# Kernel optimization log

Hardware: AMD Instinct MI355X
Metric: run time of the kernel (lower is better)

Reference implementation:

```python
import jax, jax.numpy as jnp
import numpy as np

HEADS = 12
D_MODEL = 768
D_K = D_MODEL // HEADS
BS, SEQ = 2, 4096


def setup_inputs() -> dict:
    key = jax.random.key(0)
    ks = jax.random.split(key, 12)
    s = 1.0 / np.sqrt(D_MODEL)
    return {
        "q": jax.random.normal(ks[0], (BS, SEQ, D_MODEL), jnp.float32),
        "k": jax.random.normal(ks[1], (BS, SEQ, D_MODEL), jnp.float32),
        "v": jax.random.normal(ks[2], (BS, SEQ, D_MODEL), jnp.float32),
        "Wq": jax.random.normal(ks[3], (D_MODEL, D_MODEL), jnp.float32) * s,
        "bq": jax.random.normal(ks[4], (D_MODEL,), jnp.float32) * s,
        "Wk": jax.random.normal(ks[5], (D_MODEL, D_MODEL), jnp.float32) * s,
        "bk": jax.random.normal(ks[6], (D_MODEL,), jnp.float32) * s,
        "Wv": jax.random.normal(ks[7], (D_MODEL, D_MODEL), jnp.float32) * s,
        "bv": jax.random.normal(ks[8], (D_MODEL,), jnp.float32) * s,
        "Wo": jax.random.normal(ks[9], (D_MODEL, D_MODEL), jnp.float32) * s,
        "bo": jax.random.normal(ks[10], (D_MODEL,), jnp.float32) * s,
        "mask": jnp.ones((BS, 1, SEQ), jnp.int32),
    }


def reference(q, k, v, Wq, bq, Wk, bk, Wv, bv, Wo, bo, mask):
    bs, sq, _ = q.shape
    # torch Linear: x @ W.T + b; then reshape to (bs, S, h, d_k) and transpose to (bs, h, S, d_k)
    def proj(x, W, b):
        y = x @ W.T + b
        return y.reshape(bs, -1, HEADS, D_K).transpose(0, 2, 1, 3)
    qh, kh, vh = proj(q, Wq, bq), proj(k, Wk, bk), proj(v, Wv, bv)
    scores = jnp.einsum("bhqd,bhkd->bhqk", qh, kh) / np.sqrt(D_K)
    # mask.unsqueeze(1): [bs,1,1,S_kv], masked_fill where mask == 0
    scores = jnp.where(mask[:, None, :, :] == 0, jnp.float32(-1e9), scores)
    attn = jax.nn.softmax(scores, axis=-1)  # dropout = identity (eval mode)
    ctx = jnp.einsum("bhqk,bhkd->bhqd", attn, vh)
    concat = ctx.transpose(0, 2, 1, 3).reshape(bs, sq, D_MODEL)
    return concat @ Wo.T + bo
```

## Files before the change

kernel.cpp:

```cpp
#include <hip/hip_runtime.h>
#include <hip/hip_bf16.h>

typedef __bf16 bf16x8 __attribute__((ext_vector_type(8)));
typedef __bf16 bf16x4 __attribute__((ext_vector_type(4)));
typedef short s16x4 __attribute__((ext_vector_type(4)));
typedef float f32x4 __attribute__((ext_vector_type(4)));
typedef unsigned short u16;

#define HEADS 12
#define DK 64
#define DM 768
#define SEQL 4096
#define BSZ 2
#define MROWS (BSZ * SEQL)
#define WELEM (DM * DM)
#define NX 6291456
#define WTOT (4 * WELEM)
#define BTOT (4 * 768)

#define QSCALE 0.180336880434245f
#define EXP2F(x) __builtin_amdgcn_exp2f(x)

__device__ __forceinline__ float bf2f(u16 x) {
    unsigned int u = ((unsigned int)x) << 16;
    return __uint_as_float(u);
}
__device__ __forceinline__ u16 f2bf(float f) {
    unsigned int u = __float_as_uint(f);
    u += 0x7fff + ((u >> 16) & 1);
    return (u16)(u >> 16);
}
__device__ __forceinline__ unsigned int cvt_pk(float lo, float hi) {
#if __has_builtin(__builtin_amdgcn_cvt_pk_bf16_f32)
    auto r = __builtin_amdgcn_cvt_pk_bf16_f32(lo, hi);
    unsigned int u;
    __builtin_memcpy(&u, &r, 4);
    return u;
#else
    return (unsigned int)f2bf(lo) | ((unsigned int)f2bf(hi) << 16);
#endif
}

__global__ void detect_dtype(const u16* __restrict__ q, int* __restrict__ flag) {
    __shared__ int cnt;
    if (threadIdx.x == 0) cnt = 0;
    __syncthreads();
    int c = 0;
    for (int i = threadIdx.x; i < 16384; i += 256) {
        u16 x = q[i];
        if (((x >> 7) & 0xFF) == 0xFF) c++;
    }
    if (c) atomicAdd(&cnt, c);
    __syncthreads();
    if (threadIdx.x == 0) *flag = (cnt > 0) ? 1 : 0;
}

__global__ __launch_bounds__(256) void convert_x(
    const void* __restrict__ X0, const void* __restrict__ X1, const void* __restrict__ X2,
    u16* __restrict__ Xc, const int* __restrict__ flag) {
    const int f32m = *flag;
    int i8 = blockIdx.x * 256 + threadIdx.x;
    if (i8 >= 3 * NX / 8) return;
    int w = i8 / (NX / 8);
    int off8 = i8 - w * (NX / 8);
    const void* src = (w == 0) ? X0 : (w == 1) ? X1 : X2;
    u16* dst = Xc + (size_t)w * NX + (size_t)off8 * 8;
    if (f32m) {
        float4 f0 = ((const float4*)src)[off8 * 2];
        float4 f1 = ((const float4*)src)[off8 * 2 + 1];
        uint4 p = {cvt_pk(f0.x, f0.y), cvt_pk(f0.z, f0.w),
                   cvt_pk(f1.x, f1.y), cvt_pk(f1.z, f1.w)};
        *(uint4*)dst = p;
    } else {
        *(uint4*)dst = ((const uint4*)src)[off8];
    }
}

__global__ __launch_bounds__(256) void convert_wb(
    const void* __restrict__ W0, const void* __restrict__ W1,
    const void* __restrict__ W2, const void* __restrict__ W3,
    const void* __restrict__ B0, const void* __restrict__ B1,
    const void* __restrict__ B2, const void* __restrict__ B3,
    u16* __restrict__ Wc, u16* __restrict__ bc, const int* __restrict__ flag) {
    const int f32m = *flag;
    int i4 = blockIdx.x * 256 + threadIdx.x;
    const int n4 = (WTOT + BTOT) / 4;
    if (i4 >= n4) return;
    int base = i4 * 4;
    const void* src;
    u16* dst;
    int off;
    if (base < WTOT) {
        int w = base / WELEM;
        off = base - w * WELEM;
        src = (w == 0) ? W0 : (w == 1) ? W1 : (w == 2) ? W2 : W3;
        dst = Wc + w * WELEM + off;
    } else {
        int bi = base - WTOT;
        int w = bi / 768;
        off = bi - w * 768;
        src = (w == 0) ? B0 : (w == 1) ? B1 : (w == 2) ? B2 : B3;
        dst = bc + w * 768 + off;
    }
    if (f32m) {
        float4 f = *(const float4*)((const float*)src + off);
        uint2 p = {cvt_pk(f.x, f.y), cvt_pk(f.z, f.w)};
        *(uint2*)dst = p;
    } else {
        *(uint2*)dst = *(const uint2*)((const u16*)src + off);
    }
}

typedef __attribute__((address_space(1))) unsigned int glb_u32;
typedef __attribute__((address_space(3))) unsigned int lds_u32;

__device__ __forceinline__ void gld16(const u16* g, u16* l) {
    __builtin_amdgcn_global_load_lds((glb_u32*)g, (lds_u32*)l, 16, 0, 0);
}

template <int NCH>
__device__ __forceinline__ void stage_g(const u16* gbase, u16* lbase, int tid) {
#pragma unroll
    for (int it = 0; it < NCH / 256; ++it) {
        int c = it * 256 + tid;
        int row = c >> 2, p = c & 3;
        int gc = p ^ (row & 3);
        gld16(gbase + (size_t)row * DM + gc * 8, lbase + c * 8);
    }
}

__global__ __launch_bounds__(256) void gemm_qkv3(
    const u16* __restrict__ Xc, const u16* __restrict__ Wc, const u16* __restrict__ bc,
    u16* __restrict__ Yq, u16* __restrict__ Yk, u16* __restrict__ Yv) {
    __shared__ __align__(16) u16 As[2][128 * 32];
    __shared__ __align__(16) u16 Bs[2][128 * 32];

    const int by  = blockIdx.y;
    const int sel = by / 6;
    const int n0  = (by - sel * 6) * 128;
    const int m0  = blockIdx.x * 128;

    const u16* X  = Xc + (size_t)sel * NX;
    const u16* W  = Wc + (size_t)sel * WELEM;
    const u16* Bp = bc + sel * 768;
    u16* Y = sel == 0 ? Yq : (sel == 1 ? Yk : Yv);
    const float oscale = sel == 0 ? QSCALE : 1.0f;

    const int tid = threadIdx.x, lane = tid & 63, wave = tid >> 6;
    const int wr = (wave >> 1) * 64, wc2 = (wave & 1) * 64;
    const int l15 = lane & 15, quad = lane >> 4;
    const int ck = (quad ^ (l15 & 3)) * 8;

    f32x4 acc[4][4] = {};

    stage_g<512>(X + (size_t)m0 * DM, &As[0][0], tid);
    stage_g<512>(W + (size_t)n0 * DM, &Bs[0][0], tid);
    __syncthreads();

    for (int it = 0; it < 24; ++it) {
        const int cur = it & 1, nxt = cur ^ 1;
        if (it < 23) {
            stage_g<512>(X + (size_t)m0 * DM + (it + 1) * 32, &As[nxt][0], tid);
            stage_g<512>(W + (size_t)n0 * DM + (it + 1) * 32, &Bs[nxt][0], tid);
        }
        bf16x8 a[4], b[4];
#pragma unroll
        for (int i = 0; i < 4; ++i)
            a[i] = *(const bf16x8*)&As[cur][(wr + i * 16 + l15) * 32 + ck];
#pragma unroll
        for (int j = 0; j < 4; ++j)
            b[j] = *(const bf16x8*)&Bs[cur][(wc2 + j * 16 + l15) * 32 + ck];
#pragma unroll
        for (int i = 0; i < 4; ++i)
#pragma unroll
            for (int j = 0; j < 4; ++j)
                acc[i][j] = __builtin_amdgcn_mfma_f32_16x16x32_bf16(a[i], b[j], acc[i][j], 0, 0, 0);
        __syncthreads();
    }

#pragma unroll
    for (int j = 0; j < 4; ++j) {
        int o = n0 + wc2 + j * 16 + l15;
        float bv = bf2f(Bp[o]);
        int h = o >> 6, d = o & 63;
#pragma unroll
        for (int i = 0; i < 4; ++i) {
            int row0 = m0 + wr + i * 16 + quad * 4;
            int bb = row0 >> 12, s0 = row0 & (SEQL - 1);
            if (sel < 2) {
#pragma unroll
                for (int r = 0; r < 4; ++r)
                    Y[((bb * HEADS + h) << 18) + ((s0 + r) << 6) + d] =
                        f2bf((acc[i][j][r] + bv) * oscale);
            } else {
                uint2 p = {cvt_pk(acc[i][j][0] + bv, acc[i][j][1] + bv),
                           cvt_pk(acc[i][j][2] + bv, acc[i][j][3] + bv)};
                *(uint2*)&Y[((bb * HEADS + h) << 18) + (d << 12) + s0] = p;
            }
        }
    }
}

__global__ __launch_bounds__(256) void gemm_out3(const u16* __restrict__ X,
                                                 const u16* __restrict__ W,
                                                 const u16* __restrict__ Bp,
                                                 void* __restrict__ Y,
                                                 const int* __restrict__ flag) {
    __shared__ __align__(16) u16 As[2][64 * 32];
    __shared__ __align__(16) u16 Bs[2][128 * 32];

    const int f32mode = *flag;
    const int m0 = blockIdx.x * 64, n0 = blockIdx.y * 128;
    const int tid = threadIdx.x, lane = tid & 63, wave = tid >> 6;
    const int wr = (wave >> 1) * 32, wc2 = (wave & 1) * 64;
    const int l15 = lane & 15, quad = lane >> 4;
    const int ck = (quad ^ (l15 & 3)) * 8;

    f32x4 acc[2][4] = {};

    stage_g<256>(X + (size_t)m0 * DM, &As[0][0], tid);
    stage_g<512>(W + (size_t)n0 * DM, &Bs[0][0], tid);
    __syncthreads();

    for (int it = 0; it < 24; ++it) {
        const int cur = it & 1, nxt = cur ^ 1;
        if (it < 23) {
            stage_g<256>(X + (size_t)m0 * DM + (it + 1) * 32, &As[nxt][0], tid);
            stage_g<512>(W + (size_t)n0 * DM + (it + 1) * 32, &Bs[nxt][0], tid);
        }
        bf16x8 a[2], b[4];
#pragma unroll
        for (int i = 0; i < 2; ++i)
            a[i] = *(const bf16x8*)&As[cur][(wr + i * 16 + l15) * 32 + ck];
#pragma unroll
        for (int j = 0; j < 4; ++j)
            b[j] = *(const bf16x8*)&Bs[cur][(wc2 + j * 16 + l15) * 32 + ck];
#pragma unroll
        for (int i = 0; i < 2; ++i)
#pragma unroll
            for (int j = 0; j < 4; ++j)
                acc[i][j] = __builtin_amdgcn_mfma_f32_16x16x32_bf16(a[i], b[j], acc[i][j], 0, 0, 0);
        __syncthreads();
    }

#pragma unroll
    for (int j = 0; j < 4; ++j) {
        int o = n0 + wc2 + j * 16 + l15;
        float bv = bf2f(Bp[o]);
#pragma unroll
        for (int i = 0; i < 2; ++i)
#pragma unroll
            for (int r = 0; r < 4; ++r) {
                int row = m0 + wr + i * 16 + quad * 4 + r;
                float val = acc[i][j][r] + bv;
                if (f32mode) ((float*)Y)[(size_t)row * DM + o] = val;
                else         ((u16*)Y)[(size_t)row * DM + o] = f2bf(val);
            }
    }
}

__device__ __forceinline__ void stage8_bf16(u16* dst, const u16* src) {
    *(uint4*)dst = *(const uint4*)src;
}
__device__ __forceinline__ void stage16_bf16(u16* dst, const u16* src) {
    *(uint4*)dst = *(const uint4*)src;
    *(uint4*)(dst + 8) = *(const uint4*)(src + 8);
}
__device__ __forceinline__ void stage16_f32pk(u16* dst, const float* src) {
    float4 f0 = ((const float4*)src)[0];
    float4 f1 = ((const float4*)src)[1];
    float4 f2 = ((const float4*)src)[2];
    float4 f3 = ((const float4*)src)[3];
    uint4 lo = {cvt_pk(f0.x, f0.y), cvt_pk(f0.z, f0.w), cvt_pk(f1.x, f1.y), cvt_pk(f1.z, f1.w)};
    uint4 hi = {cvt_pk(f2.x, f2.y), cvt_pk(f2.z, f2.w), cvt_pk(f3.x, f3.y), cvt_pk(f3.z, f3.w)};
    *(uint4*)dst = lo;
    *(uint4*)(dst + 8) = hi;
}

__global__ __launch_bounds__(256) void gemm_qkv_fb(
    const void* __restrict__ Xq, const void* __restrict__ Xk, const void* __restrict__ Xv,
    const u16* __restrict__ Wc, const u16* __restrict__ bc,
    u16* __restrict__ Yq, u16* __restrict__ Yk, u16* __restrict__ Yv,
    const int* __restrict__ flag) {
    __shared__ __align__(16) u16 As[128][40];
    __shared__ __align__(16) u16 Bs[64][40];
    const int f32mode = *flag;
    const int by = blockIdx.y;
    const int sel = by / 12;
    const int n0 = (by - sel * 12) * 64;
    const int m0 = blockIdx.x * 128;
    const void* Xp = sel == 0 ? Xq : (sel == 1 ? Xk : Xv);
    const u16* Wp = Wc + sel * WELEM;
    const u16* Bp = bc + sel * 768;
    u16* Y = sel == 0 ? Yq : (sel == 1 ? Yk : Yv);
    const float oscale = sel == 0 ? QSCALE : 1.0f;
    const int tid = threadIdx.x, lane = tid & 63, wave = tid >> 6;
    const int wr = (wave >> 1) * 64, wc = (wave & 1) * 32;
    const int l15 = lane & 15, quad = lane >> 4;
    const int srA = tid >> 1, scA = (tid & 1) * 16;
    const int srB = tid >> 2, scB = (tid & 3) * 8;
    f32x4 acc[4][2] = {};
    const size_t xoff = (size_t)(m0 + srA) * DM + scA;
    const size_t woff = (size_t)(n0 + srB) * DM + scB;
    for (int kb = 0; kb < DM; kb += 32) {
        if (f32mode) stage16_f32pk(&As[srA][scA], (const float*)Xp + xoff + kb);
        else         stage16_bf16(&As[srA][scA], (const u16*)Xp + xoff + kb);
        stage8_bf16(&Bs[srB][scB], Wp + woff + kb);
        __syncthreads();
        bf16x8 a[4], b[2];
#pragma unroll
        for (int i = 0; i < 4; ++i) a[i] = *(const bf16x8*)&As[wr + i * 16 + l15][quad * 8];
#pragma unroll
        for (int j = 0; j < 2; ++j) b[j] = *(const bf16x8*)&Bs[wc + j * 16 + l15][quad * 8];
#pragma unroll
        for (int i = 0; i < 4; ++i)
#pragma unroll
            for (int j = 0; j < 2; ++j)
                acc[i][j] = __builtin_amdgcn_mfma_f32_16x16x32_bf16(a[i], b[j], acc[i][j], 0, 0, 0);
        __syncthreads();
    }
#pragma unroll
    for (int j = 0; j < 2; ++j) {
        int o = n0 + wc + j * 16 + l15;
        float bv = bf2f(Bp[o]);
#pragma unroll
        for (int i = 0; i < 4; ++i)
#pragma unroll
            for (int r = 0; r < 4; ++r) {
                int row = m0 + wr + i * 16 + quad * 4 + r;
                float val = (acc[i][j][r] + bv) * oscale;
                int bb = row >> 12, s = row & (SEQL - 1);
                int h = o >> 6, d = o & 63;
                if (sel < 2) Y[((bb * HEADS + h) << 18) + (s << 6) + d] = f2bf(val);
                else         Y[((bb * HEADS + h) << 18) + (d << 12) + s] = f2bf(val);
            }
    }
}

__global__ __launch_bounds__(256) void gemm_out_fb(const u16* __restrict__ X,
                                                   const u16* __restrict__ Wp,
                                                   const u16* __restrict__ Bp,
                                                   void* __restrict__ Y,
                                                   const int* __restrict__ flag) {
    __shared__ __align__(16) u16 As[128][40];
    __shared__ __align__(16) u16 Bs[64][40];
    const int f32mode = *flag;
    const int m0 = blockIdx.x * 128, n0 = blockIdx.y * 64;
    const int tid = threadIdx.x, lane = tid & 63, wave = tid >> 6;
    const int wr = (wave >> 1) * 64, wc = (wave & 1) * 32;
    const int l15 = lane & 15, quad = lane >> 4;
    const int srA = tid >> 1, scA = (tid & 1) * 16;
    const int srB = tid >> 2, scB = (tid & 3) * 8;
    f32x4 acc[4][2] = {};
    const size_t xoff = (size_t)(m0 + srA) * DM + scA;
    const size_t woff = (size_t)(n0 + srB) * DM + scB;
    for (int kb = 0; kb < DM; kb += 32) {
        stage16_bf16(&As[srA][scA], X + xoff + kb);
        stage8_bf16(&Bs[srB][scB], Wp + woff + kb);
        __syncthreads();
        bf16x8 a[4], b[2];
#pragma unroll
        for (int i = 0; i < 4; ++i) a[i] = *(const bf16x8*)&As[wr + i * 16 + l15][quad * 8];
#pragma unroll
        for (int j = 0; j < 2; ++j) b[j] = *(const bf16x8*)&Bs[wc + j * 16 + l15][quad * 8];
#pragma unroll
        for (int i = 0; i < 4; ++i)
#pragma unroll
            for (int j = 0; j < 2; ++j)
                acc[i][j] = __builtin_amdgcn_mfma_f32_16x16x32_bf16(a[i], b[j], acc[i][j], 0, 0, 0);
        __syncthreads();
    }
#pragma unroll
    for (int j = 0; j < 2; ++j) {
        int o = n0 + wc + j * 16 + l15;
        float bv = bf2f(Bp[o]);
#pragma unroll
        for (int i = 0; i < 4; ++i)
#pragma unroll
            for (int r = 0; r < 4; ++r) {
                int row = m0 + wr + i * 16 + quad * 4 + r;
                float val = acc[i][j][r] + bv;
                if (f32mode) ((float*)Y)[(size_t)row * DM + o] = val;
                else         ((u16*)Y)[(size_t)row * DM + o] = f2bf(val);
            }
    }
}

__device__ __forceinline__ void stage_tile(const u16* gbase, int rstride,
                                           u16* lbase, int tid) {
#pragma unroll
    for (int it = 0; it < 2; ++it) {
        int c = it * 256 + tid;
        int row = c >> 3, p = c & 7;
        int gc = p ^ (row & 7);
        gld16(gbase + (size_t)row * rstride + gc * 8, lbase + c * 8);
    }
}

__global__ __launch_bounds__(256, 3) void flash_attn(const u16* __restrict__ Q,
                                                     const u16* __restrict__ K,
                                                     const u16* __restrict__ Vt,
                                                     const int* __restrict__ mask,
                                                     u16* __restrict__ ctx) {
    __shared__ __align__(16) u16 KVs[2][2][64 * 64];
    __shared__ __align__(16) float Ms[2][64];
    __shared__ int Mf[2];
    __shared__ int AnyM;

    const int tid  = threadIdx.x;
    const int lane = tid & 63;
    const int wave = tid >> 6;
    const int l15  = lane & 15;
    const int quad = lane >> 4;

    const int bh = blockIdx.y;
    const int b  = bh / HEADS;
    const int h  = bh - b * HEADS;
    const int qb = blockIdx.x * 128 + wave * 32;

    const u16* Qh = Q  + ((size_t)bh << 18);
    const u16* Kh = K  + ((size_t)bh << 18);
    const u16* Vh = Vt + ((size_t)bh << 18);
    const int* maskb = mask + b * SEQL;

    if (tid == 0) AnyM = 0;
    int zf = 0;
#pragma unroll
    for (int i = 0; i < 16; ++i) zf |= (maskb[tid + i * 256] == 0);

    bf16x8 aq[2][2];
#pragma unroll
    for (int s = 0; s < 2; ++s)
#pragma unroll
        for (int c = 0; c < 2; ++c)
            aq[s][c] = *(const bf16x8*)&Qh[(size_t)(qb + s * 16 + l15) * DK + c * 32 + quad * 8];

    __syncthreads();
    if (zf) atomicOr(&AnyM, 1);
    __syncthreads();
    const int anym = AnyM;

    const int r7   = l15 & 7;
    const int ck0  = (quad ^ r7) * 8;
    const int ck1  = ((quad + 4) ^ r7) * 8;
    const int lrow = l15 * 64;
    const int vq   = quad >> 1;
    const int voff = (quad & 1) * 4;

    float m_s[2] = {-3.0e38f, -3.0e38f};
    float l_s[2] = {0.f, 0.f};
    f32x4 o_acc[2][4] = {};

    stage_tile(Kh, DK, &KVs[0][0][0], tid);
    stage_tile(Vh, SEQL, &KVs[0][1][0], tid);
    int mreg = 0;
    if (anym && tid < 64) {
        mreg = maskb[tid];
        int anyt = __any(mreg == 0);
        Ms[0][tid] = (mreg == 0) ? -1.0e9f : 0.0f;
        if (tid == 0) Mf[0] = anyt;
        mreg = maskb[64 + tid];
    }
    __syncthreads();

#pragma unroll 2
    for (int t = 0; t < 64; ++t) {
        const int cur = t & 1, nxt = cur ^ 1;
        if (t < 63) {
            const int kt = (t + 1) * 64;
            stage_tile(Kh + (size_t)kt * DK, DK, &KVs[nxt][0][0], tid);
            stage_tile(Vh + kt, SEQL, &KVs[nxt][1][0], tid);
            if (anym && tid < 64) {
                int anyt = __any(mreg == 0);
                Ms[nxt][tid] = (mreg == 0) ? -1.0e9f : 0.0f;
                if (tid == 0) Mf[nxt] = anyt;
                if (t < 62) mreg = maskb[(t + 2) * 64 + tid];
            }
        }

        const u16* kb2 = &KVs[cur][0][0];
        const u16* vb  = &KVs[cur][1][0];

        f32x4 s4[2][4];
#pragma unroll
        for (int nt = 0; nt < 4; ++nt) {
            bf16x8 ak0 = *(const bf16x8*)&kb2[lrow + nt * 1024 + ck0];
            bf16x8 ak1 = *(const bf16x8*)&kb2[lrow + nt * 1024 + ck1];
#pragma unroll
            for (int s = 0; s < 2; ++s) {
                f32x4 z = {};
                z = __builtin_amdgcn_mfma_f32_16x16x32_bf16(ak0, aq[s][0], z, 0, 0, 0);
                z = __builtin_amdgcn_mfma_f32_16x16x32_bf16(ak1, aq[s][1], z, 0, 0, 0);
                s4[s][nt] = z;
            }
        }
        const int usebias = anym ? Mf[cur] : 0;
        if (usebias) {
#pragma unroll
            for (int nt = 0; nt < 4; ++nt) {
                f32x4 bias = *(const f32x4*)&Ms[cur][nt * 16 + quad * 4];
#pragma unroll
                for (int s = 0; s < 2; ++s)
#pragma unroll
                    for (int r = 0; r < 4; ++r) s4[s][nt][r] += bias[r];
            }
        }

        float newm[2];
#pragma unroll
        for (int s = 0; s < 2; ++s) {
            float a0 = fmaxf(fmaxf(s4[s][0][0], s4[s][0][1]), s4[s][0][2]);
            float a1 = fmaxf(fmaxf(s4[s][0][3], s4[s][1][0]), s4[s][1][1]);
            float a2 = fmaxf(fmaxf(s4[s][1][2], s4[s][1][3]), s4[s][2][0]);
            float a3 = fmaxf(fmaxf(s4[s][2][1], s4[s][2][2]), s4[s][2][3]);
            float a4 = fmaxf(fmaxf(s4[s][3][0], s4[s][3][1]), s4[s][3][2]);
            float b0 = fmaxf(fmaxf(a0, a1), a2);
            float b1 = fmaxf(fmaxf(a3, a4), s4[s][3][3]);
            float mx = fmaxf(b0, b1);
            mx = fmaxf(mx, __shfl_xor(mx, 16, 64));
            mx = fmaxf(mx, __shfl_xor(mx, 32, 64));
            newm[s] = fmaxf(m_s[s], mx);
        }

        if (!__all(newm[0] == m_s[0] && newm[1] == m_s[1])) {
#pragma unroll
            for (int s = 0; s < 2; ++s) {
                float alpha = EXP2F(m_s[s] - newm[s]);
                l_s[s] *= alpha;
#pragma unroll
                for (int dv = 0; dv < 4; ++dv) o_acc[s][dv] *= alpha;
                m_s[s] = newm[s];
            }
        }

#pragma unroll
        for (int s = 0; s < 2; ++s) {
            f32x4 ps = {};
#pragma unroll
            for (int nt = 0; nt < 4; ++nt) {
                f32x4 e = s4[s][nt] - newm[s];
                e[0] = EXP2F(e[0]); e[1] = EXP2F(e[1]);
                e[2] = EXP2F(e[2]); e[3] = EXP2F(e[3]);
                s4[s][nt] = e;
                ps += e;
            }
            l_s[s] += (ps[0] + ps[1]) + (ps[2] + ps[3]);
        }

        bf16x8 pp[2][2];
#pragma unroll
        for (int s = 0; s < 2; ++s)
#pragma unroll
            for (int kbi = 0; kbi < 2; ++kbi) {
                uint4 cv = {cvt_pk(s4[s][2 * kbi][0],     s4[s][2 * kbi][1]),
                            cvt_pk(s4[s][2 * kbi][2],     s4[s][2 * kbi][3]),
                            cvt_pk(s4[s][2 * kbi + 1][0], s4[s][2 * kbi + 1][1]),
                            cvt_pk(s4[s][2 * kbi + 1][2], s4[s][2 * kbi + 1][3])};
                __builtin_memcpy(&pp[s][kbi], &cv, 16);
            }

        bf16x8 av[4][2];
#pragma unroll
        for (int dv = 0; dv < 4; ++dv) {
            const u16* vr = &vb[(dv * 16 + l15) * 64];
#pragma unroll
            for (int kbi = 0; kbi < 2; ++kbi) {
                uint2 lo = *(const uint2*)&vr[((kbi * 4 + vq) ^ r7) * 8 + voff];
                uint2 hi = *(const uint2*)&vr[((kbi * 4 + 2 + vq) ^ r7) * 8 + voff];
                uint4 cc = {lo.x, lo.y, hi.x, hi.y};
                __builtin_memcpy(&av[dv][kbi], &cc, 16);
            }
        }

        __builtin_amdgcn_s_setprio(1);
#pragma unroll
        for (int kbi = 0; kbi < 2; ++kbi)
#pragma unroll
            for (int dv = 0; dv < 4; ++dv)
#pragma unroll
                for (int s = 0; s < 2; ++s)
                    o_acc[s][dv] = __builtin_amdgcn_mfma_f32_16x16x32_bf16(
                        av[dv][kbi], pp[s][kbi], o_acc[s][dv], 0, 0, 0);
        __builtin_amdgcn_s_setprio(0);
        __syncthreads();
    }

    u16* eb = &KVs[0][0][0] + wave * 2304;
#pragma unroll
    for (int s = 0; s < 2; ++s) {
        float lf = l_s[s];
        lf += __shfl_xor(lf, 16, 64);
        lf += __shfl_xor(lf, 32, 64);
        float inv = 1.0f / lf;
#pragma unroll
        for (int dv = 0; dv < 4; ++dv) {
            uint2 cv = {cvt_pk(o_acc[s][dv][0] * inv, o_acc[s][dv][1] * inv),
                        cvt_pk(o_acc[s][dv][2] * inv, o_acc[s][dv][3] * inv)};
            *(uint2*)&eb[(s * 16 + l15) * 72 + dv * 16 + quad * 4] = cv;
        }
    }
    asm volatile("" ::: "memory");
    {
        int rowq = lane >> 2, dchunk = lane & 3;
#pragma unroll
        for (int s = 0; s < 2; ++s) {
            uint4 w0 = *(const uint4*)&eb[(s * 16 + rowq) * 72 + dchunk * 16];
            uint4 w1 = *(const uint4*)&eb[(s * 16 + rowq) * 72 + dchunk * 16 + 8];
            size_t orow = (size_t)(b * SEQL + qb + s * 16 + rowq) * DM + h * DK + dchunk * 16;
            *(uint4*)&ctx[orow] = w0;
            *(uint4*)&ctx[orow + 8] = w1;
        }
    }
}

extern "C" void kernel_launch(void* const* d_in, const int* in_sizes, int n_in,
                              void* d_out, int out_size, void* d_ws, size_t ws_size,
                              hipStream_t stream) {
    const void* q   = d_in[0];
    const void* k   = d_in[1];
    const void* v   = d_in[2];
    const void* Wq  = d_in[3];
    const void* bq  = d_in[4];
    const void* Wk  = d_in[5];
    const void* bk  = d_in[6];
    const void* Wv  = d_in[7];
    const void* bv  = d_in[8];
    const void* Wo  = d_in[9];
    const void* bo  = d_in[10];
    const int* mask = (const int*)d_in[11];

    const size_t NSH = (size_t)NX;
    u16* ws = (u16*)d_ws;

    const size_t need_full = (6 * NSH + WTOT + BTOT) * sizeof(u16) + 64;
    const size_t need_fb   = (4 * NSH + WTOT + BTOT) * sizeof(u16) + 64;

    if (ws_size >= need_full) {
        u16* Qh  = ws;
        u16* Kh  = ws + NSH;
        u16* Vth = ws + 2 * NSH;
        u16* Xc  = ws + 3 * NSH;
        u16* ctx = Xc;
        u16* Wc  = ws + 6 * NSH;
        u16* bc  = Wc + WTOT;
        int* dflag = (int*)(bc + BTOT);

        detect_dtype<<<1, 256, 0, stream>>>((const u16*)q, dflag);
        convert_x<<<(3 * NX / 8 + 255) / 256, 256, 0, stream>>>(q, k, v, Xc, dflag);
        convert_wb<<<((WTOT + BTOT) / 4 + 255) / 256, 256, 0, stream>>>(
            Wq, Wk, Wv, Wo, bq, bk, bv, bo, Wc, bc, dflag);

        gemm_qkv3<<<dim3(MROWS / 128, 18), 256, 0, stream>>>(Xc, Wc, bc, Qh, Kh, Vth);
        flash_attn<<<dim3(SEQL / 128, BSZ * HEADS), 256, 0, stream>>>(Qh, Kh, Vth, mask, ctx);
        gemm_out3<<<dim3(MROWS / 64, 6), 256, 0, stream>>>(
            ctx, Wc + 3 * (size_t)WELEM, bc + 3 * 768, d_out, dflag);
    } else if (ws_size >= need_fb) {
        u16* Qh  = ws;
        u16* Kh  = ws + NSH;
        u16* Vth = ws + 2 * NSH;
        u16* ctx = ws + 3 * NSH;
        u16* Wc  = ws + 4 * NSH;
        u16* bc  = Wc + WTOT;
        int* dflag = (int*)(bc + BTOT);

        detect_dtype<<<1, 256, 0, stream>>>((const u16*)q, dflag);
        convert_wb<<<((WTOT + BTOT) / 4 + 255) / 256, 256, 0, stream>>>(
            Wq, Wk, Wv, Wo, bq, bk, bv, bo, Wc, bc, dflag);
        gemm_qkv_fb<<<dim3(MROWS / 128, 36), 256, 0, stream>>>(
            q, k, v, Wc, bc, Qh, Kh, Vth, dflag);
        flash_attn<<<dim3(SEQL / 128, BSZ * HEADS), 256, 0, stream>>>(Qh, Kh, Vth, mask, ctx);
        gemm_out_fb<<<dim3(MROWS / 128, 12), 256, 0, stream>>>(
            ctx, Wc + 3 * (size_t)WELEM, bc + 3 * 768, d_out, dflag);
    }
}
```

Before: 392.6 us.

## Stage QKV GEMM epilogue through LDS for coalesced stores; lazy softmax rescale

```diff
diff --git a/kernel.cpp b/kernel.cpp
--- a/kernel.cpp
+++ b/kernel.cpp
@@ -3,7 +3,6 @@
 
 typedef __bf16 bf16x8 __attribute__((ext_vector_type(8)));
 typedef __bf16 bf16x4 __attribute__((ext_vector_type(4)));
-typedef short s16x4 __attribute__((ext_vector_type(4)));
 typedef float f32x4 __attribute__((ext_vector_type(4)));
 typedef unsigned short u16;
 
@@ -130,17 +129,17 @@
 }
 
 __global__ __launch_bounds__(256) void gemm_qkv3(
-    const u16* __restrict__ Xc, const u16* __restrict__ Wc, const u16* __restrict__ bc,
+    const u16* __restrict__ X0, const u16* __restrict__ X1, const u16* __restrict__ X2,
+    const u16* __restrict__ Wc, const u16* __restrict__ bc,
     u16* __restrict__ Yq, u16* __restrict__ Yk, u16* __restrict__ Yv) {
-    __shared__ __align__(16) u16 As[2][128 * 32];
-    __shared__ __align__(16) u16 Bs[2][128 * 32];
+    __shared__ __align__(16) u16 SM[2][2][128 * 32];
 
     const int by  = blockIdx.y;
     const int sel = by / 6;
     const int n0  = (by - sel * 6) * 128;
     const int m0  = blockIdx.x * 128;
 
-    const u16* X  = Xc + (size_t)sel * NX;
+    const u16* X  = sel == 0 ? X0 : (sel == 1 ? X1 : X2);
     const u16* W  = Wc + (size_t)sel * WELEM;
     const u16* Bp = bc + sel * 768;
     u16* Y = sel == 0 ? Yq : (sel == 1 ? Yk : Yv);
@@ -153,50 +152,98 @@
 
     f32x4 acc[4][4] = {};
 
-    stage_g<512>(X + (size_t)m0 * DM, &As[0][0], tid);
-    stage_g<512>(W + (size_t)n0 * DM, &Bs[0][0], tid);
+    stage_g<512>(X + (size_t)m0 * DM, &SM[0][0][0], tid);
+    stage_g<512>(W + (size_t)n0 * DM, &SM[1][0][0], tid);
     __syncthreads();
 
     for (int it = 0; it < 24; ++it) {
         const int cur = it & 1, nxt = cur ^ 1;
         if (it < 23) {
-            stage_g<512>(X + (size_t)m0 * DM + (it + 1) * 32, &As[nxt][0], tid);
-            stage_g<512>(W + (size_t)n0 * DM + (it + 1) * 32, &Bs[nxt][0], tid);
+            stage_g<512>(X + (size_t)m0 * DM + (it + 1) * 32, &SM[0][nxt][0], tid);
+            stage_g<512>(W + (size_t)n0 * DM + (it + 1) * 32, &SM[1][nxt][0], tid);
         }
         bf16x8 a[4], b[4];
 #pragma unroll
         for (int i = 0; i < 4; ++i)
-            a[i] = *(const bf16x8*)&As[cur][(wr + i * 16 + l15) * 32 + ck];
+            a[i] = *(const bf16x8*)&SM[0][cur][(wr + i * 16 + l15) * 32 + ck];
 #pragma unroll
         for (int j = 0; j < 4; ++j)
-            b[j] = *(const bf16x8*)&Bs[cur][(wc2 + j * 16 + l15) * 32 + ck];
-#pragma unroll
-        for (int i = 0; i < 4; ++i)
-#pragma unroll
-            for (int j = 0; j < 4; ++j)
-                acc[i][j] = __builtin_amdgcn_mfma_f32_16x16x32_bf16(a[i], b[j], acc[i][j], 0, 0, 0);
+            b[j] = *(const bf16x8*)&SM[1][cur][(wc2 + j * 16 + l15) * 32 + ck];
+        if (sel < 2) {
+#pragma unroll
+            for (int i = 0; i < 4; ++i)
+#pragma unroll
+                for (int j = 0; j < 4; ++j)
+                    acc[i][j] = __builtin_amdgcn_mfma_f32_16x16x32_bf16(b[j], a[i], acc[i][j], 0, 0, 0);
+        } else {
+#pragma unroll
+            for (int i = 0; i < 4; ++i)
+#pragma unroll
+                for (int j = 0; j < 4; ++j)
+                    acc[i][j] = __builtin_amdgcn_mfma_f32_16x16x32_bf16(a[i], b[j], acc[i][j], 0, 0, 0);
+        }
         __syncthreads();
     }
 
-#pragma unroll
-    for (int j = 0; j < 4; ++j) {
-        int o = n0 + wc2 + j * 16 + l15;
-        float bv = bf2f(Bp[o]);
-        int h = o >> 6, d = o & 63;
+    u16* eb = &SM[0][0][0] + wave * 4096;
+    const int r7l = l15 & 7;
+    const int hh = (n0 + wc2) >> 6;
+
+    if (sel < 2) {
+        f32x4 bj[4];
+#pragma unroll
+        for (int j = 0; j < 4; ++j) {
+            uint2 bb4 = *(const uint2*)&Bp[n0 + wc2 + j * 16 + quad * 4];
+            bj[j][0] = bf2f((u16)(bb4.x & 0xffff));
+            bj[j][1] = bf2f((u16)(bb4.x >> 16));
+            bj[j][2] = bf2f((u16)(bb4.y & 0xffff));
+            bj[j][3] = bf2f((u16)(bb4.y >> 16));
+        }
 #pragma unroll
         for (int i = 0; i < 4; ++i) {
-            int row0 = m0 + wr + i * 16 + quad * 4;
+            int Yl = i * 16 + l15;
+#pragma unroll
+            for (int j = 0; j < 4; ++j) {
+                float v0 = (acc[i][j][0] + bj[j][0]) * oscale;
+                float v1 = (acc[i][j][1] + bj[j][1]) * oscale;
+                float v2 = (acc[i][j][2] + bj[j][2]) * oscale;
+                float v3 = (acc[i][j][3] + bj[j][3]) * oscale;
+                uint2 cv = {cvt_pk(v0, v1), cvt_pk(v2, v3)};
+                int ch = (j * 4 + quad) ^ (r7l * 2);
+                *(uint2*)&eb[Yl * 64 + ch * 4] = cv;
+            }
+        }
+        asm volatile("" ::: "memory");
+#pragma unroll
+        for (int it2 = 0; it2 < 8; ++it2) {
+            int Yp = it2 * 8 + (lane >> 3);
+            int sc = ((lane & 7) * 2) ^ ((Yp & 7) * 2);
+            uint4 w = *(const uint4*)&eb[Yp * 64 + sc * 4];
+            int row0 = m0 + wr + Yp;
             int bb = row0 >> 12, s0 = row0 & (SEQL - 1);
-            if (sel < 2) {
-#pragma unroll
-                for (int r = 0; r < 4; ++r)
-                    Y[((bb * HEADS + h) << 18) + ((s0 + r) << 6) + d] =
-                        f2bf((acc[i][j][r] + bv) * oscale);
-            } else {
-                uint2 p = {cvt_pk(acc[i][j][0] + bv, acc[i][j][1] + bv),
-                           cvt_pk(acc[i][j][2] + bv, acc[i][j][3] + bv)};
-                *(uint2*)&Y[((bb * HEADS + h) << 18) + (d << 12) + s0] = p;
-            }
+            *(uint4*)&Y[(((size_t)(bb * HEADS + hh)) << 18) + (s0 << 6) + (lane & 7) * 8] = w;
+        }
+    } else {
+#pragma unroll
+        for (int j = 0; j < 4; ++j) {
+            int Yl = j * 16 + l15;
+            float bv = bf2f(Bp[n0 + wc2 + Yl]);
+#pragma unroll
+            for (int i = 0; i < 4; ++i) {
+                uint2 cv = {cvt_pk(acc[i][j][0] + bv, acc[i][j][1] + bv),
+                            cvt_pk(acc[i][j][2] + bv, acc[i][j][3] + bv)};
+                int ch = (i * 4 + quad) ^ (r7l * 2);
+                *(uint2*)&eb[Yl * 64 + ch * 4] = cv;
+            }
+        }
+        asm volatile("" ::: "memory");
+        const int bb = (m0 + wr) >> 12, s0 = (m0 + wr) & (SEQL - 1);
+#pragma unroll
+        for (int it2 = 0; it2 < 8; ++it2) {
+            int Yp = it2 * 8 + (lane >> 3);
+            int sc = ((lane & 7) * 2) ^ ((Yp & 7) * 2);
+            uint4 w = *(const uint4*)&eb[Yp * 64 + sc * 4];
+            *(uint4*)&Y[(((size_t)(bb * HEADS + hh)) << 18) + ((size_t)Yp << 12) + s0 + (lane & 7) * 8] = w;
         }
     }
 }
@@ -494,6 +541,20 @@
                 s4[s][nt] = z;
             }
         }
+
+        bf16x8 av[4][2];
+#pragma unroll
+        for (int dv = 0; dv < 4; ++dv) {
+            const u16* vr = &vb[(dv * 16 + l15) * 64];
+#pragma unroll
+            for (int kbi = 0; kbi < 2; ++kbi) {
+                uint2 lo = *(const uint2*)&vr[((kbi * 4 + vq) ^ r7) * 8 + voff];
+                uint2 hi = *(const uint2*)&vr[((kbi * 4 + 2 + vq) ^ r7) * 8 + voff];
+                uint4 cc = {lo.x, lo.y, hi.x, hi.y};
+                __builtin_memcpy(&av[dv][kbi], &cc, 16);
+            }
+        }
+
         const int usebias = anym ? Mf[cur] : 0;
         if (usebias) {
 #pragma unroll
@@ -506,7 +567,7 @@
             }
         }
 
-        float newm[2];
+        float mx2[2];
 #pragma unroll
         for (int s = 0; s < 2; ++s) {
             float a0 = fmaxf(fmaxf(s4[s][0][0], s4[s][0][1]), s4[s][0][2]);
@@ -519,17 +580,18 @@
             float mx = fmaxf(b0, b1);
             mx = fmaxf(mx, __shfl_xor(mx, 16, 64));
             mx = fmaxf(mx, __shfl_xor(mx, 32, 64));
-            newm[s] = fmaxf(m_s[s], mx);
-        }
-
-        if (!__all(newm[0] == m_s[0] && newm[1] == m_s[1])) {
+            mx2[s] = mx;
+        }
+
+        if (!__all((mx2[0] <= m_s[0] + 8.f) && (mx2[1] <= m_s[1] + 8.f))) {
 #pragma unroll
             for (int s = 0; s < 2; ++s) {
-                float alpha = EXP2F(m_s[s] - newm[s]);
+                float newm = fmaxf(m_s[s], mx2[s]);
+                float alpha = EXP2F(m_s[s] - newm);
                 l_s[s] *= alpha;
 #pragma unroll
                 for (int dv = 0; dv < 4; ++dv) o_acc[s][dv] *= alpha;
-                m_s[s] = newm[s];
+                m_s[s] = newm;
             }
         }
 
@@ -538,7 +600,7 @@
             f32x4 ps = {};
 #pragma unroll
             for (int nt = 0; nt < 4; ++nt) {
-                f32x4 e = s4[s][nt] - newm[s];
+                f32x4 e = s4[s][nt] - m_s[s];
                 e[0] = EXP2F(e[0]); e[1] = EXP2F(e[1]);
                 e[2] = EXP2F(e[2]); e[3] = EXP2F(e[3]);
                 s4[s][nt] = e;
@@ -558,19 +620,6 @@
                             cvt_pk(s4[s][2 * kbi + 1][2], s4[s][2 * kbi + 1][3])};
                 __builtin_memcpy(&pp[s][kbi], &cv, 16);
             }
-
-        bf16x8 av[4][2];
-#pragma unroll
-        for (int dv = 0; dv < 4; ++dv) {
-            const u16* vr = &vb[(dv * 16 + l15) * 64];
-#pragma unroll
-            for (int kbi = 0; kbi < 2; ++kbi) {
-                uint2 lo = *(const uint2*)&vr[((kbi * 4 + vq) ^ r7) * 8 + voff];
-                uint2 hi = *(const uint2*)&vr[((kbi * 4 + 2 + vq) ^ r7) * 8 + voff];
-                uint4 cc = {lo.x, lo.y, hi.x, hi.y};
-                __builtin_memcpy(&av[dv][kbi], &cc, 16);
-            }
-        }
 
         __builtin_amdgcn_s_setprio(1);
 #pragma unroll
@@ -650,7 +699,8 @@
         convert_wb<<<((WTOT + BTOT) / 4 + 255) / 256, 256, 0, stream>>>(
             Wq, Wk, Wv, Wo, bq, bk, bv, bo, Wc, bc, dflag);
 
-        gemm_qkv3<<<dim3(MROWS / 128, 18), 256, 0, stream>>>(Xc, Wc, bc, Qh, Kh, Vth);
+        gemm_qkv3<<<dim3(MROWS / 128, 18), 256, 0, stream>>>(
+            Xc, Xc + NSH, Xc + 2 * NSH, Wc, bc, Qh, Kh, Vth);
         flash_attn<<<dim3(SEQL / 128, BSZ * HEADS), 256, 0, stream>>>(Qh, Kh, Vth, mask, ctx);
         gemm_out3<<<dim3(MROWS / 64, 6), 256, 0, stream>>>(
             ctx, Wc + 3 * (size_t)WELEM, bc + 3 * 768, d_out, dflag);
```

Measured after the change: 402.2 us. 2.4% more time.
